# Kernel optimization log

Hardware: AMD Instinct MI355X
Metric: run time of the kernel (lower is better)

Reference implementation:

```python
import jax, jax.numpy as jnp
import numpy as np

NEG_SLOPE = 0.2  # PyG GATConv default leaky_relu slope


def add_self_loops(edge_index, n):
    ar = jnp.arange(n, dtype=edge_index.dtype)
    loops = jnp.stack([ar, ar])
    return jnp.concatenate([edge_index, loops], axis=1)


def gat_conv(x, edge_index, W, a_src, a_dst, bias, heads, out_ch, concat):
    # x: [N, F_in]; edge_index: [2, E] with row0=src(j), row1=dst(i)
    N = x.shape[0]
    src, dst = edge_index[0], edge_index[1]
    h = (x @ W).reshape(N, heads, out_ch)            # [N, H, C]
    alpha_s = jnp.einsum('nhc,hc->nh', h, a_src)     # [N, H]
    alpha_d = jnp.einsum('nhc,hc->nh', h, a_dst)
    e = jax.nn.leaky_relu(alpha_s[src] + alpha_d[dst], NEG_SLOPE)  # [E, H]
    # segment softmax over incoming edges of each dst node
    e_max = jax.ops.segment_max(e, dst, num_segments=N)           # [N, H]
    e_exp = jnp.exp(e - e_max[dst])
    denom = jax.ops.segment_sum(e_exp, dst, num_segments=N)       # [N, H]
    alpha = e_exp / denom[dst]                                     # [E, H]
    msg = h[src] * alpha[:, :, None]                               # [E, H, C]
    out = jax.ops.segment_sum(msg, dst, num_segments=N)           # [N, H, C]
    out = out.reshape(N, heads * out_ch) if concat else out.mean(axis=1)
    return out + bias


def setup_inputs() -> dict:
    key = jax.random.key(0)
    ks = jax.random.split(key, 10)
    N, F_in, E, C_out = 100000, 256, 1600000, 100
    H1, D1 = 8, 8
    x = jax.random.normal(ks[0], (N, F_in), dtype=jnp.float32)
    edge_index = jax.random.randint(ks[1], (2, E), 0, N, dtype=jnp.int64)
    s = 0.1
    return {
        'x': x,
        'edge_index': edge_index,
        'W1': jax.random.normal(ks[2], (F_in, H1 * D1), dtype=jnp.float32) * s,
        'a_src1': jax.random.normal(ks[3], (H1, D1), dtype=jnp.float32) * s,
        'a_dst1': jax.random.normal(ks[4], (H1, D1), dtype=jnp.float32) * s,
        'b1': jnp.zeros((H1 * D1,), dtype=jnp.float32),
        'W2': jax.random.normal(ks[5], (H1 * D1, C_out), dtype=jnp.float32) * s,
        'a_src2': jax.random.normal(ks[6], (1, C_out), dtype=jnp.float32) * s,
        'a_dst2': jax.random.normal(ks[7], (1, C_out), dtype=jnp.float32) * s,
        'b2': jnp.zeros((C_out,), dtype=jnp.float32),
    }


def reference(x, edge_index, W1, a_src1, a_dst1, b1, W2, a_src2, a_dst2, b2):
    N = x.shape[0]
    ei = add_self_loops(edge_index, N)
    # dropout layers are identity in eval mode
    h = jax.nn.elu(gat_conv(x, ei, W1, a_src1, a_dst1, b1, heads=8, out_ch=8, concat=True))
    out = gat_conv(h, ei, W2, a_src2, a_dst2, b2, heads=1, out_ch=W2.shape[1], concat=False)
    return jax.nn.sigmoid(out)
```

## Files before the change

### kernel.cpp

```cpp
#include <hip/hip_runtime.h>
#include <hip/hip_bf16.h>
#include <cmath>


#define BSH 9
#define BNN (1 << BSH)
#define SEG 12288

typedef __attribute__((ext_vector_type(8))) short short8v;
typedef __attribute__((ext_vector_type(4))) float f32x4;

__device__ __forceinline__ float lrelu02(float v) { return v > 0.f ? v : 0.2f * v; }

__device__ __forceinline__ unsigned short f2b(float f) {
  union { float f; unsigned int i; } c; c.f = f;
  unsigned int r = c.i + 0x7FFFu + ((c.i >> 16) & 1u);
  return (unsigned short)(r >> 16);
}
__device__ __forceinline__ float lo16(unsigned int u) {
  union { float f; unsigned int i; } c; c.i = u << 16; return c.f;
}
__device__ __forceinline__ float hi16(unsigned int u) {
  union { float f; unsigned int i; } c; c.i = u & 0xFFFF0000u; return c.f;
}


__global__ __launch_bounds__(256) void k_init(const float* __restrict__ W1,
                                              unsigned short* __restrict__ w1t,
                                              const float* __restrict__ W2,
                                              const float* __restrict__ a2s,
                                              const float* __restrict__ a2d,
                                              float* __restrict__ w2as, float* __restrict__ w2ad,
                                              int* __restrict__ bcur0, int K,
                                              int* __restrict__ offs, int N, int E) {
  int b = blockIdx.x, t = threadIdx.x;
  if (b < 16) {
    int idx = b * 256 + t;
#pragma unroll
    for (int j = 0; j < 4; ++j) {
      int e = idx * 4 + j;
      int col = e >> 8, k = e & 255;
      w1t[e] = f2b(W1[k * 64 + col]);
    }
  } else {
    if (t < K) bcur0[t] = 0;
    if (t == 255) offs[N] = E + N;
    if (t < 64) {
      float s = 0.f;
      for (int k = 0; k < 100; ++k) s += W2[t * 100 + k] * a2s[k];
      w2as[t] = s;
    } else if (t < 128) {
      int c = t - 64;
      float s = 0.f;
      for (int k = 0; k < 100; ++k) s += W2[c * 100 + k] * a2d[k];
      w2ad[c] = s;
    }
  }
}


__device__ __forceinline__ void gemm1_body(const float* __restrict__ x,
                                           const unsigned short* __restrict__ w1t,
                                           const float* __restrict__ av_s,
                                           const float* __restrict__ av_d,
                                           unsigned short* __restrict__ h1b,
                                           float* __restrict__ as1, float* __restrict__ ad1,
                                           int N, int row0, unsigned short* xs ) {
  int tid = threadIdx.x;
  int w = tid >> 6, lane = tid & 63;
  int wr = w & 1, wc = w >> 1;
  int r16 = lane & 15, kg4 = lane >> 4;
  const unsigned short* pw = &w1t[(32 * wc + r16) * 256 + kg4 * 8];
  short8v breg[8][2];
#pragma unroll
  for (int ks = 0; ks < 8; ++ks) {
#pragma unroll
    for (int f = 0; f < 2; ++f) {
      union { short8v s; uint4 u; } bv;
      bv.u = *(const uint4*)(pw + f * 16 * 256 + ks * 32);
      breg[ks][f] = bv.s;
    }
  }
#pragma unroll
  for (int it = 0; it < 4; ++it) {
    int slot = tid + it * 256;
    int row = slot >> 5, kg = slot & 31;
    int grow = row0 + row;
    uint4 pk = make_uint4(0u, 0u, 0u, 0u);
    if (grow < N) {
      const float* px = &x[(size_t)grow * 256 + kg * 8];
      float4 v0 = *(const float4*)px;
      float4 v1 = *(const float4*)(px + 4);
      pk.x = f2b(v0.x) | ((unsigned)f2b(v0.y) << 16);
      pk.y = f2b(v0.z) | ((unsigned)f2b(v0.w) << 16);
      pk.z = f2b(v1.x) | ((unsigned)f2b(v1.y) << 16);
      pk.w = f2b(v1.z) | ((unsigned)f2b(v1.w) << 16);
    }
    *(uint4*)&xs[row * 268 + kg * 8] = pk;
  }
  __syncthreads();
  f32x4 acc[2];
  acc[0] = (f32x4){0.f, 0.f, 0.f, 0.f};
  acc[1] = (f32x4){0.f, 0.f, 0.f, 0.f};
  const unsigned short* xrow = &xs[(16 * wr + r16) * 268 + kg4 * 8];
#pragma unroll
  for (int ks = 0; ks < 8; ++ks) {
    short8v a = *(const short8v*)(xrow + ks * 32);
    acc[0] = __builtin_amdgcn_mfma_f32_16x16x32_bf16(a, breg[ks][0], acc[0], 0, 0, 0);
    acc[1] = __builtin_amdgcn_mfma_f32_16x16x32_bf16(a, breg[ks][1], acc[1], 0, 0, 0);
  }
  float avv[2], bvv[2];
#pragma unroll
  for (int f = 0; f < 2; ++f) {
    avv[f] = av_s[32 * wc + 16 * f + r16];
    bvv[f] = av_d[32 * wc + 16 * f + r16];
  }
  int rbase = row0 + 16 * wr + kg4 * 4;
#pragma unroll
  for (int reg = 0; reg < 4; ++reg) {
    int row = rbase + reg;
    bool ok = row < N;
    if (ok) {
#pragma unroll
      for (int f = 0; f < 2; ++f)
        h1b[(size_t)row * 64 + 32 * wc + 16 * f + r16] = f2b(acc[f][reg]);
    }
    float ts[2], td[2];
#pragma unroll
    for (int f = 0; f < 2; ++f) { ts[f] = acc[f][reg] * avv[f]; td[f] = acc[f][reg] * bvv[f]; }
#pragma unroll
    for (int off = 1; off <= 4; off <<= 1) {
#pragma unroll
      for (int f = 0; f < 2; ++f) {
        ts[f] += __shfl_xor(ts[f], off);
        td[f] += __shfl_xor(td[f], off);
      }
    }
    if (ok && (r16 & 7) == 0) {
      int bsel = r16 >> 3;
#pragma unroll
      for (int f = 0; f < 2; ++f) {
        as1[row * 8 + 4 * wc + 2 * f + bsel] = ts[f];
        ad1[row * 8 + 4 * wc + 2 * f + bsel] = td[f];
      }
    }
  }
}


__global__ __launch_bounds__(256) void k_g1bin(const float* __restrict__ x,
                                               const unsigned short* __restrict__ w1t,
                                               const float* __restrict__ av_s, const float* __restrict__ av_d,
                                               unsigned short* __restrict__ h1b,
                                               float* __restrict__ as1, float* __restrict__ ad1,
                                               int N, int GA,
                                               const int* __restrict__ ei, int E,
                                               int* __restrict__ bcur0, unsigned int* __restrict__ binned2) {
  __shared__ unsigned short xs[32 * 268];
  if ((int)blockIdx.x < GA) {
    gemm1_body(x, w1t, av_s, av_d, h1b, as1, ad1, N, blockIdx.x * 32, xs);
    return;
  }
  int* lh = (int*)xs;
  int* lbase = lh + 256;
  int tid = threadIdx.x;
  lh[tid] = 0;
  __syncthreads();
  int base = (blockIdx.x - GA) * 2048;
  int bj[8], rk[8];
  unsigned int pk[8];
#pragma unroll
  for (int j = 0; j < 8; ++j) {
    int e = base + j * 256 + tid;
    bj[j] = -1;
    if (e < E) {
      unsigned int sj = (unsigned int)ei[e];
      int d = ei[E + e];
      bj[j] = d >> BSH;
      pk[j] = sj | ((unsigned int)(d & (BNN - 1)) << 17);
      rk[j] = atomicAdd(&lh[bj[j]], 1);
    }
  }
  __syncthreads();
  if (lh[tid]) lbase[tid] = atomicAdd(&bcur0[tid], lh[tid]);
  __syncthreads();
#pragma unroll
  for (int j = 0; j < 8; ++j)
    if (bj[j] >= 0) binned2[(size_t)bj[j] * SEG + lbase[bj[j]] + rk[j]] = pk[j];
}


__global__ __launch_bounds__(256) void k_g1bkt(const float* __restrict__ x,
                                               const unsigned short* __restrict__ w1t,
                                               const float* __restrict__ av_s, const float* __restrict__ av_d,
                                               unsigned short* __restrict__ h1b,
                                               float* __restrict__ as1, float* __restrict__ ad1,
                                               int N, int rowbase, int GB,
                                               const int* __restrict__ bcur0,
                                               const unsigned int* __restrict__ binned2,
                                               int* __restrict__ offs, int* __restrict__ csr, int K) {
  __shared__ unsigned short xs[32 * 268];
  if ((int)blockIdx.x < GB) {
    gemm1_body(x, w1t, av_s, av_d, h1b, as1, ad1, N, rowbase + blockIdx.x * 32, xs);
    return;
  }
  int* hist  = (int*)xs;
  int* loffS = hist + BNN;
  int* cur   = loffS + BNN;
  int* s     = cur + BNN;
  __shared__ int sh_e0, sh_cnt;
  int tid = threadIdx.x;
  int b = blockIdx.x - GB;
  int node0 = b << BSH;
  int sl = min(BNN, N - node0);
  int v = (tid < K) ? bcur0[tid] : 0;
  s[tid] = v;
  __syncthreads();
  for (int off = 1; off < 256; off <<= 1) {
    int t = (tid >= off) ? s[tid - off] : 0;
    __syncthreads();
    s[tid] += t;
    __syncthreads();
  }
  if (tid == b) { sh_e0 = s[tid] - v; sh_cnt = v; }
  __syncthreads();
  int e0 = sh_e0, cnt = sh_cnt;
  int cbase = e0 + min(node0, N);
  const unsigned int* seg = &binned2[(size_t)b * SEG];
  hist[tid] = 0; hist[tid + 256] = 0;
  __syncthreads();
  for (int e = tid; e < cnt; e += 256) atomicAdd(&hist[seg[e] >> 17], 1);
  __syncthreads();
  int a0 = hist[2 * tid], a1 = hist[2 * tid + 1];
  s[tid] = a0 + a1;
  __syncthreads();
  for (int off = 1; off < 256; off <<= 1) {
    int t = (tid >= off) ? s[tid - off] : 0;
    __syncthreads();
    s[tid] += t;
    __syncthreads();
  }
  int excl = s[tid] - (a0 + a1);
  loffS[2 * tid]     = excl + 2 * tid;
  loffS[2 * tid + 1] = excl + a0 + 2 * tid + 1;
  __syncthreads();
  cur[2 * tid] = loffS[2 * tid];
  cur[2 * tid + 1] = loffS[2 * tid + 1];
  if (2 * tid < sl)     offs[node0 + 2 * tid]     = cbase + loffS[2 * tid];
  if (2 * tid + 1 < sl) offs[node0 + 2 * tid + 1] = cbase + loffS[2 * tid + 1];
  __syncthreads();
  for (int e = tid; e < cnt; e += 256) {
    unsigned int u = seg[e];
    int p = atomicAdd(&cur[u >> 17], 1);
    csr[cbase + p] = (int)(u & 0x1FFFFu);
  }
  for (int i = tid; i < sl; i += 256) {
    int p = atomicAdd(&cur[i], 1);
    csr[cbase + p] = node0 + i;
  }
}


__global__ __launch_bounds__(256) void k_agg1(const int* __restrict__ csr, const int* __restrict__ offs,
                                              const unsigned short* __restrict__ h1b,
                                              const float* __restrict__ as1, const float* __restrict__ ad1,
                                              const float* __restrict__ b1,
                                              const float* __restrict__ w2as, const float* __restrict__ w2ad,
                                              unsigned short* __restrict__ helu_b,
                                              float* __restrict__ as2, float* __restrict__ ad2, int N) {
  __shared__ float wsm[4][8][8][9];
  int tid = threadIdx.x;
  int w = tid >> 6, lane = tid & 63;
  int sub = lane >> 3, q = lane & 7;
  int base = sub << 3;
  int node = blockIdx.x * 32 + w * 8 + sub;
  bool valid = node < N;
  int beg = 0, end = 0;
  if (valid) { beg = offs[node]; end = offs[node + 1]; }
  int deg = end - beg;
  int dm = deg;
  dm = max(dm, __shfl_xor(dm, 8));
  dm = max(dm, __shfl_xor(dm, 16));
  dm = max(dm, __shfl_xor(dm, 32));
  float4 advlo = make_float4(0.f, 0.f, 0.f, 0.f), advhi = advlo;
  if (valid) {
    advlo = *(const float4*)&ad1[node * 8];
    advhi = *(const float4*)&ad1[node * 8 + 4];
  }
  float denom = 0.f;
  float4 acc0 = make_float4(0.f, 0.f, 0.f, 0.f);
  float4 acc1 = make_float4(0.f, 0.f, 0.f, 0.f);
  for (int c0 = 0; c0 < dm; c0 += 8) {
    int cn = min(8, deg - c0);
    int sreg = 0;
    if (q < cn) {
      sreg = csr[beg + c0 + q];
      float4 alo = *(const float4*)&as1[sreg * 8];
      float4 ahi = *(const float4*)&as1[sreg * 8 + 4];
      wsm[w][sub][0][q] = __expf(lrelu02(alo.x + advlo.x));
      wsm[w][sub][1][q] = __expf(lrelu02(alo.y + advlo.y));
      wsm[w][sub][2][q] = __expf(lrelu02(alo.z + advlo.z));
      wsm[w][sub][3][q] = __expf(lrelu02(alo.w + advlo.w));
      wsm[w][sub][4][q] = __expf(lrelu02(ahi.x + advhi.x));
      wsm[w][sub][5][q] = __expf(lrelu02(ahi.y + advhi.y));
      wsm[w][sub][6][q] = __expf(lrelu02(ahi.z + advhi.z));
      wsm[w][sub][7][q] = __expf(lrelu02(ahi.w + advhi.w));
    }
    int i = 0;
    for (; i + 2 <= cn; i += 2) {
      int s0 = __shfl(sreg, base + i);
      int s1 = __shfl(sreg, base + i + 1);
      float w0 = wsm[w][sub][q][i];
      float w1 = wsm[w][sub][q][i + 1];
      uint4 p0 = *(const uint4*)&h1b[(unsigned)s0 * 64 + q * 8];
      uint4 p1 = *(const uint4*)&h1b[(unsigned)s1 * 64 + q * 8];
      denom += w0 + w1;
      acc0.x += w0 * lo16(p0.x); acc0.y += w0 * hi16(p0.x);
      acc0.z += w0 * lo16(p0.y); acc0.w += w0 * hi16(p0.y);
      acc1.x += w0 * lo16(p0.z); acc1.y += w0 * hi16(p0.z);
      acc1.z += w0 * lo16(p0.w); acc1.w += w0 * hi16(p0.w);
      acc0.x += w1 * lo16(p1.x); acc0.y += w1 * hi16(p1.x);
      acc0.z += w1 * lo16(p1.y); acc0.w += w1 * hi16(p1.y);
      acc1.x += w1 * lo16(p1.z); acc1.y += w1 * hi16(p1.z);
      acc1.z += w1 * lo16(p1.w); acc1.w += w1 * hi16(p1.w);
    }
    if (i < cn) {
      int s0 = __shfl(sreg, base + i);
      float w0 = wsm[w][sub][q][i];
      uint4 p0 = *(const uint4*)&h1b[(unsigned)s0 * 64 + q * 8];
      denom += w0;
      acc0.x += w0 * lo16(p0.x); acc0.y += w0 * hi16(p0.x);
      acc0.z += w0 * lo16(p0.y); acc0.w += w0 * hi16(p0.y);
      acc1.x += w0 * lo16(p0.z); acc1.y += w0 * hi16(p0.z);
      acc1.z += w0 * lo16(p0.w); acc1.w += w0 * hi16(p0.w);
    }
  }
  float rd = 1.f / denom;
  float4 ba = valid ? *(const float4*)&b1[q * 8] : make_float4(0.f, 0.f, 0.f, 0.f);
  float4 bb = valid ? *(const float4*)&b1[q * 8 + 4] : make_float4(0.f, 0.f, 0.f, 0.f);
  float o[8];
  o[0] = acc0.x * rd + ba.x; o[1] = acc0.y * rd + ba.y;
  o[2] = acc0.z * rd + ba.z; o[3] = acc0.w * rd + ba.w;
  o[4] = acc1.x * rd + bb.x; o[5] = acc1.y * rd + bb.y;
  o[6] = acc1.z * rd + bb.z; o[7] = acc1.w * rd + bb.w;
#pragma unroll
  for (int j = 0; j < 8; ++j) o[j] = o[j] > 0.f ? o[j] : __expf(o[j]) - 1.f;
  if (valid) {
    uint4 ob;
    ob.x = f2b(o[0]) | ((unsigned)f2b(o[1]) << 16);
    ob.y = f2b(o[2]) | ((unsigned)f2b(o[3]) << 16);
    ob.z = f2b(o[4]) | ((unsigned)f2b(o[5]) << 16);
    ob.w = f2b(o[6]) | ((unsigned)f2b(o[7]) << 16);
    *(uint4*)&helu_b[(size_t)node * 64 + q * 8] = ob;
  }
  float s2 = 0.f, d2 = 0.f;
  if (valid) {
    float4 wa0 = *(const float4*)&w2as[q * 8];
    float4 wa1 = *(const float4*)&w2as[q * 8 + 4];
    float4 wd0 = *(const float4*)&w2ad[q * 8];
    float4 wd1 = *(const float4*)&w2ad[q * 8 + 4];
    s2 = o[0] * wa0.x + o[1] * wa0.y + o[2] * wa0.z + o[3] * wa0.w
       + o[4] * wa1.x + o[5] * wa1.y + o[6] * wa1.z + o[7] * wa1.w;
    d2 = o[0] * wd0.x + o[1] * wd0.y + o[2] * wd0.z + o[3] * wd0.w
       + o[4] * wd1.x + o[5] * wd1.y + o[6] * wd1.z + o[7] * wd1.w;
  }
#pragma unroll
  for (int off = 1; off <= 4; off <<= 1) {
    s2 += __shfl_xor(s2, off);
    d2 += __shfl_xor(d2, off);
  }
  if (valid && q == 0) { as2[node] = s2; ad2[node] = d2; }
}


__global__ __launch_bounds__(256) void k_agg2(const int* __restrict__ csr, const int* __restrict__ offs,
                                              const unsigned short* __restrict__ helu_b,
                                              const float* __restrict__ as2, const float* __restrict__ ad2,
                                              unsigned short* __restrict__ aggb, int N) {
  int tid = threadIdx.x;
  int lane = tid & 63;
  int sub = lane >> 3, q = lane & 7;
  int base = sub << 3;
  int node = blockIdx.x * 32 + (tid >> 6) * 8 + sub;
  bool valid = node < N;
  int beg = 0, end = 0;
  if (valid) { beg = offs[node]; end = offs[node + 1]; }
  int deg = end - beg;
  int dm = deg;
  dm = max(dm, __shfl_xor(dm, 8));
  dm = max(dm, __shfl_xor(dm, 16));
  dm = max(dm, __shfl_xor(dm, 32));
  float adv = valid ? ad2[node] : 0.f;
  float denom = 0.f;
  float4 acc0 = make_float4(0.f, 0.f, 0.f, 0.f);
  float4 acc1 = make_float4(0.f, 0.f, 0.f, 0.f);
  for (int c0 = 0; c0 < dm; c0 += 8) {
    int cn = min(8, deg - c0);
    int sreg = 0; float wq = 0.f;
    if (q < cn) {
      sreg = csr[beg + c0 + q];
      wq = __expf(lrelu02(as2[sreg] + adv));
    }
    int i = 0;
    for (; i + 2 <= cn; i += 2) {
      int s0 = __shfl(sreg, base + i);
      int s1 = __shfl(sreg, base + i + 1);
      float w0 = __shfl(wq, base + i);
      float w1 = __shfl(wq, base + i + 1);
      uint4 p0 = *(const uint4*)&helu_b[(unsigned)s0 * 64 + q * 8];
      uint4 p1 = *(const uint4*)&helu_b[(unsigned)s1 * 64 + q * 8];
      denom += w0 + w1;
      acc0.x += w0 * lo16(p0.x); acc0.y += w0 * hi16(p0.x);
      acc0.z += w0 * lo16(p0.y); acc0.w += w0 * hi16(p0.y);
      acc1.x += w0 * lo16(p0.z); acc1.y += w0 * hi16(p0.z);
      acc1.z += w0 * lo16(p0.w); acc1.w += w0 * hi16(p0.w);
      acc0.x += w1 * lo16(p1.x); acc0.y += w1 * hi16(p1.x);
      acc0.z += w1 * lo16(p1.y); acc0.w += w1 * hi16(p1.y);
      acc1.x += w1 * lo16(p1.z); acc1.y += w1 * hi16(p1.z);
      acc1.z += w1 * lo16(p1.w); acc1.w += w1 * hi16(p1.w);
    }
    if (i < cn) {
      int s0 = __shfl(sreg, base + i);
      float w0 = __shfl(wq, base + i);
      uint4 p0 = *(const uint4*)&helu_b[(unsigned)s0 * 64 + q * 8];
      denom += w0;
      acc0.x += w0 * lo16(p0.x); acc0.y += w0 * hi16(p0.x);
      acc0.z += w0 * lo16(p0.y); acc0.w += w0 * hi16(p0.y);
      acc1.x += w0 * lo16(p0.z); acc1.y += w0 * hi16(p0.z);
      acc1.z += w0 * lo16(p0.w); acc1.w += w0 * hi16(p0.w);
    }
  }
  if (valid) {
    float rd = 1.f / denom;
    uint4 ob;
    ob.x = f2b(acc0.x * rd) | ((unsigned)f2b(acc0.y * rd) << 16);
    ob.y = f2b(acc0.z * rd) | ((unsigned)f2b(acc0.w * rd) << 16);
    ob.z = f2b(acc1.x * rd) | ((unsigned)f2b(acc1.y * rd) << 16);
    ob.w = f2b(acc1.z * rd) | ((unsigned)f2b(acc1.w * rd) << 16);
    *(uint4*)&aggb[(size_t)node * 64 + q * 8] = ob;
  }
}


__global__ __launch_bounds__(256) void k_gemm2b(const unsigned short* __restrict__ aggb,
                                                const float* __restrict__ W2,
                                                const float* __restrict__ b2, float* __restrict__ out, int N) {
  __shared__ float het[64][44];
  __shared__ float w2l[64 * 100];
  int tid = threadIdx.x;
  int row0 = blockIdx.x * 40;
  for (int i = tid; i < 6400; i += 256) w2l[i] = W2[i];
  for (int idx = tid; idx < 640; idx += 256) {
    int r = idx >> 4, kq = idx & 15;
    int grow = row0 + r;
    uint2 v = make_uint2(0u, 0u);
    if (grow < N) v = *(const uint2*)&aggb[(size_t)grow * 64 + kq * 4];
    het[kq * 4 + 0][r] = lo16(v.x); het[kq * 4 + 1][r] = hi16(v.x);
    het[kq * 4 + 2][r] = lo16(v.y); het[kq * 4 + 3][r] = hi16(v.y);
  }
  __syncthreads();
  int rg = tid / 25, cg = tid % 25;
  if (rg >= 10) return;
  float acc[4][4] = {};
#pragma unroll 4
  for (int k = 0; k < 64; ++k) {
    float4 xv = *(const float4*)&het[k][rg * 4];
    float4 wv = *(const float4*)&w2l[k * 100 + cg * 4];
    float xa[4] = {xv.x, xv.y, xv.z, xv.w};
    float wa[4] = {wv.x, wv.y, wv.z, wv.w};
#pragma unroll
    for (int i = 0; i < 4; ++i)
#pragma unroll
      for (int j = 0; j < 4; ++j) acc[i][j] += xa[i] * wa[j];
  }
  float bb[4];
#pragma unroll
  for (int j = 0; j < 4; ++j) bb[j] = b2[cg * 4 + j];
#pragma unroll
  for (int i = 0; i < 4; ++i) {
    int row = row0 + rg * 4 + i;
    if (row < N) {
      float4 o;
      o.x = 1.f / (1.f + __expf(-(acc[i][0] + bb[0])));
      o.y = 1.f / (1.f + __expf(-(acc[i][1] + bb[1])));
      o.z = 1.f / (1.f + __expf(-(acc[i][2] + bb[2])));
      o.w = 1.f / (1.f + __expf(-(acc[i][3] + bb[3])));
      *(float4*)&out[(size_t)row * 100 + cg * 4] = o;
    }
  }
}


extern "C" void kernel_launch(void* const* d_in, const int* in_sizes, int n_in,
                              void* d_out, int out_size, void* d_ws, size_t ws_size,
                              hipStream_t stream) {
  const float* x    = (const float*)d_in[0];
  const int*   ei   = (const int*)d_in[1];
  const float* W1   = (const float*)d_in[2];
  const float* a_s1 = (const float*)d_in[3];
  const float* a_d1 = (const float*)d_in[4];
  const float* b1   = (const float*)d_in[5];
  const float* W2   = (const float*)d_in[6];
  const float* a_s2 = (const float*)d_in[7];
  const float* a_d2 = (const float*)d_in[8];
  const float* b2   = (const float*)d_in[9];
  float* out = (float*)d_out;

  const int N = in_sizes[0] / 256;
  const int E = in_sizes[1] / 2;
  const int K = (N + BNN - 1) >> BSH;

  char* w = (char*)d_ws;
  size_t off = 0;
  auto alloc = [&](size_t bytes) -> char* {
    char* p = w + off;
    off = (off + bytes + 255) & ~(size_t)255;
    return p;
  };
  unsigned short* h1b    = (unsigned short*)alloc((size_t)N * 64 * 2);
  unsigned short* helu_b = (unsigned short*)alloc((size_t)N * 64 * 2);
  unsigned short* aggb   = (unsigned short*)alloc((size_t)N * 64 * 2);
  unsigned short* w1t    = (unsigned short*)alloc(64 * 256 * 2);
  float* as1  = (float*)alloc((size_t)N * 8 * 4);
  float* ad1  = (float*)alloc((size_t)N * 8 * 4);
  float* as2  = (float*)alloc((size_t)N * 4);
  float* ad2  = (float*)alloc((size_t)N * 4);
  float* w2as = (float*)alloc(64 * 4);
  float* w2ad = (float*)alloc(64 * 4);
  int*   offs   = (int*)alloc((size_t)(N + 1) * 4);
  int*   csr    = (int*)alloc((size_t)(E + N) * 4);
  unsigned int* binned2 = (unsigned int*)alloc((size_t)K * SEG * 4);
  int*   bcur0  = (int*)alloc((size_t)K * 4);
  (void)ws_size; (void)n_in; (void)out_size;

  k_init<<<17, 256, 0, stream>>>(W1, w1t, W2, a_s2, a_d2, w2as, w2ad, bcur0, K, offs, N, E);

  const int ebl = (E + 2047) / 2048;
  const int totalG = (N + 31) / 32;
  const int GA = (totalG + 1) / 2;
  const int GB = totalG - GA;
  const int rowbase = GA * 32;

  k_g1bin<<<GA + ebl, 256, 0, stream>>>(x, w1t, a_s1, a_d1, h1b, as1, ad1, N, GA,
                                        ei, E, bcur0, binned2);
  k_g1bkt<<<GB + K, 256, 0, stream>>>(x, w1t, a_s1, a_d1, h1b, as1, ad1, N, rowbase, GB,
                                      bcur0, binned2, offs, csr, K);

  k_agg1<<<(N + 31) / 32, 256, 0, stream>>>(csr, offs, h1b, as1, ad1, b1, w2as, w2ad,
                                            helu_b, as2, ad2, N);
  k_agg2<<<(N + 31) / 32, 256, 0, stream>>>(csr, offs, helu_b, as2, ad2, aggb, N);
  k_gemm2b<<<(N + 39) / 40, 256, 0, stream>>>(aggb, W2, b2, out, N);
}
```

Measured before the change: 206.3 us.

## Fuse layer-2 aggregation with output GEMM using bf16 MFMA in LDS

Merges the layer-2 aggregation kernel and the final 64x100 projection GEMM into one kernel. Aggregated rows stay in shared memory as bf16 and are multiplied by a pre-transposed, padded bf16 W2 using 16x16x32 MFMA instructions, then bias and sigmoid are applied. This removes the aggb global round trip (N*64 bf16 written and read back) and one launch, and moves the small GEMM from FP32 FMAs to matrix cores. In exchange, output stores are scalar and strided per column, W2 is read from global memory inside each tile, and precision drops to bf16 for W2.

Result: faster. 199.7 us (-3.2%).

```diff
diff --git a/kernel.cpp b/kernel.cpp
--- a/kernel.cpp
+++ b/kernel.cpp
@@ -31,6 +31,7 @@
                                               const float* __restrict__ a2s,
                                               const float* __restrict__ a2d,
                                               float* __restrict__ w2as, float* __restrict__ w2ad,
+                                              unsigned short* __restrict__ w2t,
                                               int* __restrict__ bcur0, int K,
                                               int* __restrict__ offs, int N, int E) {
   int b = blockIdx.x, t = threadIdx.x;
@@ -54,6 +55,10 @@
       float s = 0.f;
       for (int k = 0; k < 100; ++k) s += W2[c * 100 + k] * a2d[k];
       w2ad[c] = s;
+    }
+    for (int i = t; i < 112 * 64; i += 256) {
+      int c = i >> 6, k = i & 63;
+      w2t[i] = f2b(c < 100 ? W2[k * 100 + c] : 0.f);
     }
   }
 }
@@ -373,15 +378,19 @@
 }
 
 
-__global__ __launch_bounds__(256) void k_agg2(const int* __restrict__ csr, const int* __restrict__ offs,
-                                              const unsigned short* __restrict__ helu_b,
-                                              const float* __restrict__ as2, const float* __restrict__ ad2,
-                                              unsigned short* __restrict__ aggb, int N) {
+__global__ __launch_bounds__(256) void k_agg2g(const int* __restrict__ csr, const int* __restrict__ offs,
+                                               const unsigned short* __restrict__ helu_b,
+                                               const float* __restrict__ as2, const float* __restrict__ ad2,
+                                               const unsigned short* __restrict__ w2t,
+                                               const float* __restrict__ b2,
+                                               float* __restrict__ out, int N) {
+  __shared__ unsigned short aggl[32 * 68];
   int tid = threadIdx.x;
-  int lane = tid & 63;
+  int w = tid >> 6, lane = tid & 63;
   int sub = lane >> 3, q = lane & 7;
   int base = sub << 3;
-  int node = blockIdx.x * 32 + (tid >> 6) * 8 + sub;
+  int nb = w * 8 + sub;
+  int node = blockIdx.x * 32 + nb;
   bool valid = node < N;
   int beg = 0, end = 0;
   if (valid) { beg = offs[node]; end = offs[node + 1]; }
@@ -430,62 +439,37 @@
       acc1.z += w0 * lo16(p0.w); acc1.w += w0 * hi16(p0.w);
     }
   }
-  if (valid) {
-    float rd = 1.f / denom;
-    uint4 ob;
-    ob.x = f2b(acc0.x * rd) | ((unsigned)f2b(acc0.y * rd) << 16);
-    ob.y = f2b(acc0.z * rd) | ((unsigned)f2b(acc0.w * rd) << 16);
-    ob.z = f2b(acc1.x * rd) | ((unsigned)f2b(acc1.y * rd) << 16);
-    ob.w = f2b(acc1.z * rd) | ((unsigned)f2b(acc1.w * rd) << 16);
-    *(uint4*)&aggb[(size_t)node * 64 + q * 8] = ob;
-  }
-}
-
-
-__global__ __launch_bounds__(256) void k_gemm2b(const unsigned short* __restrict__ aggb,
-                                                const float* __restrict__ W2,
-                                                const float* __restrict__ b2, float* __restrict__ out, int N) {
-  __shared__ float het[64][44];
-  __shared__ float w2l[64 * 100];
-  int tid = threadIdx.x;
-  int row0 = blockIdx.x * 40;
-  for (int i = tid; i < 6400; i += 256) w2l[i] = W2[i];
-  for (int idx = tid; idx < 640; idx += 256) {
-    int r = idx >> 4, kq = idx & 15;
-    int grow = row0 + r;
-    uint2 v = make_uint2(0u, 0u);
-    if (grow < N) v = *(const uint2*)&aggb[(size_t)grow * 64 + kq * 4];
-    het[kq * 4 + 0][r] = lo16(v.x); het[kq * 4 + 1][r] = hi16(v.x);
-    het[kq * 4 + 2][r] = lo16(v.y); het[kq * 4 + 3][r] = hi16(v.y);
-  }
-  __syncthreads();
-  int rg = tid / 25, cg = tid % 25;
-  if (rg >= 10) return;
-  float acc[4][4] = {};
-#pragma unroll 4
-  for (int k = 0; k < 64; ++k) {
-    float4 xv = *(const float4*)&het[k][rg * 4];
-    float4 wv = *(const float4*)&w2l[k * 100 + cg * 4];
-    float xa[4] = {xv.x, xv.y, xv.z, xv.w};
-    float wa[4] = {wv.x, wv.y, wv.z, wv.w};
-#pragma unroll
-    for (int i = 0; i < 4; ++i)
-#pragma unroll
-      for (int j = 0; j < 4; ++j) acc[i][j] += xa[i] * wa[j];
-  }
-  float bb[4];
-#pragma unroll
-  for (int j = 0; j < 4; ++j) bb[j] = b2[cg * 4 + j];
-#pragma unroll
-  for (int i = 0; i < 4; ++i) {
-    int row = row0 + rg * 4 + i;
-    if (row < N) {
-      float4 o;
-      o.x = 1.f / (1.f + __expf(-(acc[i][0] + bb[0])));
-      o.y = 1.f / (1.f + __expf(-(acc[i][1] + bb[1])));
-      o.z = 1.f / (1.f + __expf(-(acc[i][2] + bb[2])));
-      o.w = 1.f / (1.f + __expf(-(acc[i][3] + bb[3])));
-      *(float4*)&out[(size_t)row * 100 + cg * 4] = o;
+  float rd = valid ? (1.f / denom) : 0.f;
+  uint4 ob;
+  ob.x = f2b(acc0.x * rd) | ((unsigned)f2b(acc0.y * rd) << 16);
+  ob.y = f2b(acc0.z * rd) | ((unsigned)f2b(acc0.w * rd) << 16);
+  ob.z = f2b(acc1.x * rd) | ((unsigned)f2b(acc1.y * rd) << 16);
+  ob.w = f2b(acc1.z * rd) | ((unsigned)f2b(acc1.w * rd) << 16);
+  *(uint4*)&aggl[nb * 68 + q * 8] = ob;
+  __syncthreads();
+  int r16 = lane & 15, kg4 = lane >> 4;
+#pragma unroll
+  for (int tt = 0; tt < 4; ++tt) {
+    int t = w + tt * 4;
+    if (t >= 14) break;
+    int m = t & 1, n = t >> 1;
+    f32x4 cacc = (f32x4){0.f, 0.f, 0.f, 0.f};
+#pragma unroll
+    for (int ks = 0; ks < 2; ++ks) {
+      short8v a = *(const short8v*)&aggl[(16 * m + r16) * 68 + ks * 32 + kg4 * 8];
+      short8v b = *(const short8v*)&w2t[(16 * n + r16) * 64 + ks * 32 + kg4 * 8];
+      cacc = __builtin_amdgcn_mfma_f32_16x16x32_bf16(a, b, cacc, 0, 0, 0);
+    }
+    int col = 16 * n + r16;
+    if (col < 100) {
+      float bc = b2[col];
+      int rowb = 16 * m + kg4 * 4;
+#pragma unroll
+      for (int reg = 0; reg < 4; ++reg) {
+        int onode = blockIdx.x * 32 + rowb + reg;
+        if (onode < N)
+          out[(size_t)onode * 100 + col] = 1.f / (1.f + __expf(-(cacc[reg] + bc)));
+      }
     }
   }
 }
@@ -519,8 +503,8 @@
   };
   unsigned short* h1b    = (unsigned short*)alloc((size_t)N * 64 * 2);
   unsigned short* helu_b = (unsigned short*)alloc((size_t)N * 64 * 2);
-  unsigned short* aggb   = (unsigned short*)alloc((size_t)N * 64 * 2);
   unsigned short* w1t    = (unsigned short*)alloc(64 * 256 * 2);
+  unsigned short* w2t    = (unsigned short*)alloc(112 * 64 * 2);
   float* as1  = (float*)alloc((size_t)N * 8 * 4);
   float* ad1  = (float*)alloc((size_t)N * 8 * 4);
   float* as2  = (float*)alloc((size_t)N * 4);
@@ -533,7 +517,8 @@
   int*   bcur0  = (int*)alloc((size_t)K * 4);
   (void)ws_size; (void)n_in; (void)out_size;
 
-  k_init<<<17, 256, 0, stream>>>(W1, w1t, W2, a_s2, a_d2, w2as, w2ad, bcur0, K, offs, N, E);
+  k_init<<<17, 256, 0, stream>>>(W1, w1t, W2, a_s2, a_d2, w2as, w2ad, w2t,
+                                 bcur0, K, offs, N, E);
 
   const int ebl = (E + 2047) / 2048;
   const int totalG = (N + 31) / 32;
@@ -548,6 +533,5 @@
 
   k_agg1<<<(N + 31) / 32, 256, 0, stream>>>(csr, offs, h1b, as1, ad1, b1, w2as, w2ad,
                                             helu_b, as2, ad2, N);
-  k_agg2<<<(N + 31) / 32, 256, 0, stream>>>(csr, offs, helu_b, as2, ad2, aggb, N);
-  k_gemm2b<<<(N + 39) / 40, 256, 0, stream>>>(aggb, W2, b2, out, N);
-}
+  k_agg2g<<<(N + 31) / 32, 256, 0, stream>>>(csr, offs, helu_b, as2, ad2, w2t, b2, out, N);
+}
```
